# Kernel tuning notes

Measured on AMD Instinct MI355X. Metric: run time of the kernel, lower is better.

## Reference

```python
import jax, jax.numpy as jnp
import numpy as np

IMG = 64            # image_height = image_width = 64
NPTS = 300          # n_pts_per_ray
MIN_DEPTH, MAX_DEPTH = 0.1, 3.0
GRID = 16           # latent_dim -> 16^3 voxel grid
VOXEL_SIZE = 0.1
FOV_DEG = 60.0      # pytorch3d FoVPerspectiveCameras default
B = 8               # number of cameras / latents
EPS = 1e-10         # EmissionAbsorptionRaymarcher eps


def _look_at(eye, at):
    # pytorch3d look_at_view_transform: row-vector convention x_view = x_world @ R + T
    up = np.array([0.0, 1.0, 0.0])
    z = at - eye; z = z / np.linalg.norm(z)
    x = np.cross(up, z); x = x / np.linalg.norm(x)
    y = np.cross(z, x); y = y / np.linalg.norm(y)
    R = np.stack([x, y, z], axis=1)  # columns are camera axes
    T = -eye @ R
    return R, T


def setup_inputs():
    rng = np.random.default_rng(0)
    Rs, Ts = [], []
    for _ in range(B):
        eye = rng.standard_normal(3) * np.array([0.01, 0.0001, 0.01])
        at = rng.standard_normal(3) * 0.01
        R, T = _look_at(eye, at)
        Rs.append(R); Ts.append(T)

    def lin(fan_in, fan_out):
        bound = 1.0 / np.sqrt(fan_in)  # torch Linear default init
        W = rng.uniform(-bound, bound, size=(fan_in, fan_out))
        b = rng.uniform(-bound, bound, size=(fan_out,))
        return jnp.asarray(W, jnp.float32), jnp.asarray(b, jnp.float32)

    W1, b1 = lin(30, 60)
    W2, b2 = lin(60, 480)
    W3, b3 = lin(480, 4 * GRID ** 3)
    zs = jnp.asarray(rng.standard_normal((B, 30)), jnp.float32)
    return {"zs": zs, "W1": W1, "b1": b1, "W2": W2, "b2": b2, "W3": W3, "b3": b3,
            "R": jnp.asarray(np.stack(Rs), jnp.float32),
            "T": jnp.asarray(np.stack(Ts), jnp.float32)}


def _grid_sample3d(vol, xyz):
    # vol: (C, D, H, W); xyz: (..., 3) in [-1, 1]; trilinear, align_corners=True, zero padding
    C, D, H, W = vol.shape
    batch_shape = xyz.shape[:-1]
    p = xyz.reshape(-1, 3)
    ix = (p[:, 0] + 1.0) * 0.5 * (W - 1)
    iy = (p[:, 1] + 1.0) * 0.5 * (H - 1)
    iz = (p[:, 2] + 1.0) * 0.5 * (D - 1)
    x0 = jnp.floor(ix); y0 = jnp.floor(iy); z0 = jnp.floor(iz)
    tx = ix - x0; ty = iy - y0; tz = iz - z0
    out = jnp.zeros((C, p.shape[0]), vol.dtype)
    for dx, wx in ((0, 1.0 - tx), (1, tx)):
        for dy, wy in ((0, 1.0 - ty), (1, ty)):
            for dz, wz in ((0, 1.0 - tz), (1, tz)):
                xf, yf, zf = x0 + dx, y0 + dy, z0 + dz
                valid = ((xf >= 0) & (xf <= W - 1) & (yf >= 0) & (yf <= H - 1)
                         & (zf >= 0) & (zf <= D - 1))
                xi = jnp.clip(xf, 0, W - 1).astype(jnp.int32)
                yi = jnp.clip(yf, 0, H - 1).astype(jnp.int32)
                zi = jnp.clip(zf, 0, D - 1).astype(jnp.int32)
                w = jnp.where(valid, wx * wy * wz, 0.0)
                out = out + w[None, :] * vol[:, zi, yi, xi]
    return jnp.moveaxis(out.reshape((C,) + batch_shape), 0, -1)


def _forward(zs, W1, b1, W2, b2, W3, b3, R, T):
    # latent MLP -> (B, 4, 16, 16, 16) volume (1 density channel + 3 color channels)
    h = jax.nn.sigmoid(zs @ W1 + b1)
    h = jax.nn.sigmoid(h @ W2 + b2)
    lat = jax.nn.sigmoid(h @ W3 + b3).reshape(-1, 4, GRID, GRID, GRID)
    densities = lat[:, 0:1]   # (B,1,D,H,W)
    colors = lat[:, 1:4]      # (B,3,D,H,W)

    # NDCGridRaysampler pixel-center grid (pytorch3d NDC: +x left, +y up, row 0 at max y)
    half_pix = 1.0 / IMG
    xs = jnp.linspace(1.0 - half_pix, -1.0 + half_pix, IMG)
    ys = jnp.linspace(1.0 - half_pix, -1.0 + half_pix, IMG)
    f = 1.0 / jnp.tan(jnp.deg2rad(FOV_DEG) / 2.0)  # focal from fov, aspect=1
    dir_cam = jnp.stack([jnp.broadcast_to(xs[None, :] / f, (IMG, IMG)),
                         jnp.broadcast_to(ys[:, None] / f, (IMG, IMG)),
                         jnp.ones((IMG, IMG))], axis=-1)  # (H,W,3)
    Rt = jnp.swapaxes(R, 1, 2)                             # view->world rotation
    dirs_w = jnp.einsum('hwc,bcd->bhwd', dir_cam, Rt)      # (B,H,W,3)
    origins_w = jnp.einsum('bc,bcd->bd', -T, Rt)           # camera centers (B,3)

    depths = jnp.linspace(MIN_DEPTH, MAX_DEPTH, NPTS)
    pts = origins_w[:, None, None, None, :] + dirs_w[:, :, :, None, :] * depths[None, None, None, :, None]
    half_extent = (GRID - 1) * VOXEL_SIZE * 0.5            # pytorch3d Volumes world->local scale
    local = pts / half_extent                              # (B,H,W,P,3)

    sigma = jax.vmap(_grid_sample3d)(densities, local)[..., 0]  # (B,H,W,P)
    feats = jax.vmap(_grid_sample3d)(colors, local)             # (B,H,W,P,3)

    # EmissionAbsorptionRaymarcher (surface_thickness=1)
    a = (1.0 + EPS) - sigma
    cp = jnp.cumprod(a, axis=-1)
    absorption = jnp.concatenate([jnp.ones_like(cp[..., :1]), cp[..., :-1]], axis=-1)
    weights = sigma * absorption
    rgb = jnp.sum(weights[..., None] * feats, axis=-2)          # (B,H,W,3)
    opacity = 1.0 - jnp.prod(1.0 - sigma, axis=-1, keepdims=True)
    return jnp.concatenate([rgb, opacity], axis=-1)             # (B,H,W,4)


def reference(zs, W1, b1, W2, b2, W3, b3, R, T):
    imgs = _forward(zs, W1, b1, W2, b2, W3, b3, R, T)
    return imgs[..., 3:4], imgs[..., 0:3]
```

## Files before the change

kernel.cpp:

```cpp
#include <hip/hip_runtime.h>
#include <hip/hip_bf16.h>

#define IMG 64
#define NPTS 300
#define GRIDN 16
#define BATCH 8

typedef __hip_bfloat16 bf16;

__device__ __forceinline__ float sigm(float x) { return 1.0f / (1.0f + __expf(-x)); }
__device__ __forceinline__ float lo_bf(unsigned u) { return __uint_as_float(u << 16); }
__device__ __forceinline__ float hi_bf(unsigned u) { return __uint_as_float(u & 0xffff0000u); }

template <typename T>
__device__ __forceinline__ float ldv(const void* p, int i);
template <>
__device__ __forceinline__ float ldv<float>(const void* p, int i) { return ((const float*)p)[i]; }
template <>
__device__ __forceinline__ float ldv<bf16>(const void* p, int i) {
    return __bfloat162float(((const bf16*)p)[i]);
}

__device__ __forceinline__ void sniff(const void* W1, int* sflag, int t) {
    if (t < 64) {
        float m = 0.0f;
        for (int i = t; i < 1800; i += 64) {
            float v = fabsf(__bfloat162float(((const bf16*)W1)[i]));
            if (!(v < 1e30f)) v = 1e30f;
            m = fmaxf(m, v);
        }
#pragma unroll
        for (int d = 1; d < 64; d <<= 1) m = fmaxf(m, __shfl_xor(m, d));
        if (t == 0) *sflag = (m > 4.0f) ? 1 : 0;
    }
}

template <typename T>
__device__ void prep_body(const void* zs, const void* b1, const void* W1, const void* W2,
                          const void* b2, const void* W3, const void* b3,
                          bf16* __restrict__ volbf) {
    __shared__ float z[BATCH][30];
    __shared__ float h1[BATCH][60];
    __shared__ __align__(16) float h2[BATCH][480];
    int t = threadIdx.x;

    if (t < 240) {
        int b = t / 30, i = t - b * 30;
        z[b][i] = ldv<T>(zs, t);
    }
    __syncthreads();
    if (t < 480) {
        int b = t / 60, j = t - b * 60;
        float acc = ldv<T>(b1, j);
#pragma unroll
        for (int i = 0; i < 30; ++i) acc = fmaf(z[b][i], ldv<T>(W1, i * 60 + j), acc);
        h1[b][j] = sigm(acc);
    }
    __syncthreads();
    for (int idx = t; idx < BATCH * 480; idx += 512) {
        int b = idx / 480, col = idx - b * 480;
        float acc = ldv<T>(b2, col);
#pragma unroll
        for (int i = 0; i < 60; ++i) acc = fmaf(h1[b][i], ldv<T>(W2, i * 480 + col), acc);
        h2[b][col] = sigm(acc);
    }
    __syncthreads();

    int b = t >> 6;
    int j = blockIdx.x * 64 + (t & 63);
    float acc = ldv<T>(b3, j);
#pragma unroll 2
    for (int i = 0; i < 480; i += 8) {
        float4 ha = *(const float4*)&h2[b][i];
        float4 hb = *(const float4*)&h2[b][i + 4];
        acc = fmaf(ha.x, ldv<T>(W3, (size_t)(i + 0) * 16384 + j), acc);
        acc = fmaf(ha.y, ldv<T>(W3, (size_t)(i + 1) * 16384 + j), acc);
        acc = fmaf(ha.z, ldv<T>(W3, (size_t)(i + 2) * 16384 + j), acc);
        acc = fmaf(ha.w, ldv<T>(W3, (size_t)(i + 3) * 16384 + j), acc);
        acc = fmaf(hb.x, ldv<T>(W3, (size_t)(i + 4) * 16384 + j), acc);
        acc = fmaf(hb.y, ldv<T>(W3, (size_t)(i + 5) * 16384 + j), acc);
        acc = fmaf(hb.z, ldv<T>(W3, (size_t)(i + 6) * 16384 + j), acc);
        acc = fmaf(hb.w, ldv<T>(W3, (size_t)(i + 7) * 16384 + j), acc);
    }
    float a = sigm(acc);
    int c = j >> 12, v = j & 4095;
    volbf[(size_t)(((b << 12) + v) << 2) + c] = __float2bfloat16(a);
}

__global__ __launch_bounds__(512) void prep_kernel(const void* zs, const void* W1,
                                                   const void* b1, const void* W2,
                                                   const void* b2, const void* W3,
                                                   const void* b3, bf16* __restrict__ volbf,
                                                   int* __restrict__ flag) {
    __shared__ int sflag;
    int t = threadIdx.x;
    sniff(W1, &sflag, t);
    __syncthreads();
    if (blockIdx.x == 0 && t == 0) *flag = sflag;
    if (sflag)
        prep_body<float>(zs, b1, W1, W2, b2, W3, b3, volbf);
    else
        prep_body<bf16>(zs, b1, W1, W2, b2, W3, b3, volbf);
}

__global__ __launch_bounds__(256) void render_kernel(const void* Rm, const void* Tm,
                                                     const bf16* __restrict__ volbf, void* out,
                                                     const int* __restrict__ flag) {
    __shared__ uint2 vox[4096];
    int t = threadIdx.x;
    int rayBase = blockIdx.x * 64;
    int b = rayBase >> 12;
    const uint2* src = (const uint2*)(volbf + (size_t)b * 4096 * 4);
    for (int i = t; i < 4096; i += 256) vox[i] = src[i];
    __syncthreads();

    int f32out = *flag;
    int ray = rayBase + (t >> 2);
    int seg = t & 3;
    int pix = ray & 4095;
    int h = pix >> 6, w = pix & 63;

    const float inv_f = 0.57735026919f;
    float dcx = (0.984375f - 0.03125f * (float)w) * inv_f;
    float dcy = (0.984375f - 0.03125f * (float)h) * inv_f;

    float R[9], Tv[3];
    if (f32out) {
#pragma unroll
        for (int i = 0; i < 9; ++i) R[i] = ((const float*)Rm)[b * 9 + i];
#pragma unroll
        for (int i = 0; i < 3; ++i) Tv[i] = ((const float*)Tm)[b * 3 + i];
    } else {
#pragma unroll
        for (int i = 0; i < 9; ++i) R[i] = __bfloat162float(((const bf16*)Rm)[b * 9 + i]);
#pragma unroll
        for (int i = 0; i < 3; ++i) Tv[i] = __bfloat162float(((const bf16*)Tm)[b * 3 + i]);
    }

    float dx_ = dcx * R[0] + dcy * R[1] + R[2];
    float dy_ = dcx * R[3] + dcy * R[4] + R[5];
    float dz_ = dcx * R[6] + dcy * R[7] + R[8];
    float ox = -(Tv[0] * R[0] + Tv[1] * R[1] + Tv[2] * R[2]);
    float oy = -(Tv[0] * R[3] + Tv[1] * R[4] + Tv[2] * R[5]);
    float oz = -(Tv[0] * R[6] + Tv[1] * R[7] + Tv[2] * R[8]);

    float tA = -1e30f, tB = 1e30f;
    bool miss = false;
    {
        float dd[3] = {dx_, dy_, dz_}, oo[3] = {ox, oy, oz};
#pragma unroll
        for (int a = 0; a < 3; ++a) {
            if (fabsf(dd[a]) > 1e-8f) {
                float inv = 1.0f / dd[a];
                float ra = (-0.85f - oo[a]) * inv, rb = (0.85f - oo[a]) * inv;
                tA = fmaxf(tA, fminf(ra, rb));
                tB = fminf(tB, fmaxf(ra, rb));
            } else if (fabsf(oo[a]) >= 0.85f) {
                miss = true;
            }
        }
    }
    const float step = 2.9f / 299.0f;
    const float inv_step = 299.0f / 2.9f;
    int ilo = 0, ihi = -1;
    if (!miss && tB > tA) {
        float flo = fmaxf(-2.0f, fminf(302.0f, ceilf((tA - 0.1f) * inv_step)));
        float fhi = fmaxf(-2.0f, fminf(302.0f, floorf((tB - 0.1f) * inv_step)));
        ilo = (int)flo - 1;
        ihi = (int)fhi + 1;
        if (ilo < 0) ilo = 0;
        if (ihi > 299) ihi = 299;
    }
    int n = ihi - ilo + 1;
    if (n < 0) n = 0;
    int s0 = ilo + (n * seg) / 4;
    int s1 = ilo + (n * (seg + 1)) / 4;

    float cr = 0.f, cg = 0.f, cb = 0.f, Pa = 1.f;
    for (int i = s0; i < s1; ++i) {
        float tt = 0.1f + step * (float)i;
        float ix = fmaf(fmaf(tt, dx_, ox), 10.0f, 7.5f);
        float iy = fmaf(fmaf(tt, dy_, oy), 10.0f, 7.5f);
        float iz = fmaf(fmaf(tt, dz_, oz), 10.0f, 7.5f);
        float fx = floorf(ix), fy = floorf(iy), fz = floorf(iz);
        float txf = ix - fx, tyf = iy - fy, tzf = iz - fz;
        int x0 = (int)fx, y0 = (int)fy, z0 = (int)fz;

        float sx = 0.f, sr = 0.f, sg = 0.f, sb = 0.f;
        if (((unsigned)x0 < 15u) & ((unsigned)y0 < 15u) & ((unsigned)z0 < 15u)) {
            int base = (z0 << 8) + (y0 << 4) + x0;
            float wx0 = 1.0f - txf, wy0 = 1.0f - tyf, wz0 = 1.0f - tzf;
            float wxy00 = wx0 * wy0, wxy10 = txf * wy0, wxy01 = wx0 * tyf, wxy11 = txf * tyf;
#define CORNF(W, OFF)                          \
    {                                          \
        uint2 q = vox[base + (OFF)];           \
        float wgt_ = (W);                      \
        sx = fmaf(wgt_, lo_bf(q.x), sx);       \
        sr = fmaf(wgt_, hi_bf(q.x), sr);       \
        sg = fmaf(wgt_, lo_bf(q.y), sg);       \
        sb = fmaf(wgt_, hi_bf(q.y), sb);       \
    }
            CORNF(wxy00 * wz0, 0)
            CORNF(wxy10 * wz0, 1)
            CORNF(wxy01 * wz0, 16)
            CORNF(wxy11 * wz0, 17)
            CORNF(wxy00 * tzf, 256)
            CORNF(wxy10 * tzf, 257)
            CORNF(wxy01 * tzf, 272)
            CORNF(wxy11 * tzf, 273)
#undef CORNF
        } else {
            float wx0 = (x0 >= 0 && x0 <= 15) ? (1.0f - txf) : 0.0f;
            float wx1 = (x0 >= -1 && x0 <= 14) ? txf : 0.0f;
            float wy0 = (y0 >= 0 && y0 <= 15) ? (1.0f - tyf) : 0.0f;
            float wy1 = (y0 >= -1 && y0 <= 14) ? tyf : 0.0f;
            float wz0 = (z0 >= 0 && z0 <= 15) ? (1.0f - tzf) : 0.0f;
            float wz1 = (z0 >= -1 && z0 <= 14) ? tzf : 0.0f;
            int xi0 = min(max(x0, 0), 15), xi1 = min(max(x0 + 1, 0), 15);
            int yi0 = min(max(y0, 0), 15), yi1 = min(max(y0 + 1, 0), 15);
            int zi0 = min(max(z0, 0), 15), zi1 = min(max(z0 + 1, 0), 15);
#define CORN(W, ZI, YI, XI)                              \
    {                                                    \
        uint2 q = vox[((ZI) << 8) + ((YI) << 4) + (XI)]; \
        sx = fmaf((W), lo_bf(q.x), sx);                  \
        sr = fmaf((W), hi_bf(q.x), sr);                  \
        sg = fmaf((W), lo_bf(q.y), sg);                  \
        sb = fmaf((W), hi_bf(q.y), sb);                  \
    }
            float wxy00 = wx0 * wy0, wxy10 = wx1 * wy0, wxy01 = wx0 * wy1, wxy11 = wx1 * wy1;
            CORN(wxy00 * wz0, zi0, yi0, xi0)
            CORN(wxy10 * wz0, zi0, yi0, xi1)
            CORN(wxy01 * wz0, zi0, yi1, xi0)
            CORN(wxy11 * wz0, zi0, yi1, xi1)
            CORN(wxy00 * wz1, zi1, yi0, xi0)
            CORN(wxy10 * wz1, zi1, yi0, xi1)
            CORN(wxy01 * wz1, zi1, yi1, xi0)
            CORN(wxy11 * wz1, zi1, yi1, xi1)
#undef CORN
        }

        float wgt = sx * Pa;
        cr = fmaf(wgt, sr, cr);
        cg = fmaf(wgt, sg, cg);
        cb = fmaf(wgt, sb, cb);
        Pa *= (1.0f - sx);
    }

#pragma unroll
    for (int d = 1; d < 4; d <<= 1) {
        float o_cr = __shfl_xor(cr, d);
        float o_cg = __shfl_xor(cg, d);
        float o_cb = __shfl_xor(cb, d);
        float o_Pa = __shfl_xor(Pa, d);
        bool first = ((seg & d) == 0);
        cr = first ? fmaf(Pa, o_cr, cr) : fmaf(o_Pa, cr, o_cr);
        cg = first ? fmaf(Pa, o_cg, cg) : fmaf(o_Pa, cg, o_cg);
        cb = first ? fmaf(Pa, o_cb, cb) : fmaf(o_Pa, cb, o_cb);
        Pa *= o_Pa;
    }

    if (seg == 0) {
        if (f32out) {
            float* of = (float*)out;
            of[ray] = 1.0f - Pa;
            float* orgb = of + BATCH * IMG * IMG;
            orgb[ray * 3 + 0] = cr;
            orgb[ray * 3 + 1] = cg;
            orgb[ray * 3 + 2] = cb;
        } else {
            bf16* ob = (bf16*)out;
            ob[ray] = __float2bfloat16(1.0f - Pa);
            bf16* orgb = ob + BATCH * IMG * IMG;
            orgb[ray * 3 + 0] = __float2bfloat16(cr);
            orgb[ray * 3 + 1] = __float2bfloat16(cg);
            orgb[ray * 3 + 2] = __float2bfloat16(cb);
        }
    }
}

extern "C" void kernel_launch(void* const* d_in, const int* in_sizes, int n_in,
                              void* d_out, int out_size, void* d_ws, size_t ws_size,
                              hipStream_t stream) {
    const void* zs = d_in[0];
    const void* W1 = d_in[1];
    const void* b1 = d_in[2];
    const void* W2 = d_in[3];
    const void* b2 = d_in[4];
    const void* W3 = d_in[5];
    const void* b3 = d_in[6];
    const void* Rm = d_in[7];
    const void* Tm = d_in[8];

    bf16* volbf = (bf16*)d_ws;
    int* flag = (int*)((char*)d_ws + 262144);

    hipLaunchKernelGGL(prep_kernel, dim3(256), dim3(512), 0, stream, zs, W1, b1, W2, b2, W3,
                       b3, volbf, flag);
    hipLaunchKernelGGL(render_kernel, dim3(512), dim3(256), 0, stream, Rm, Tm, volbf, d_out,
                       flag);
}
```

Baseline: 141.0 us.

## Split W3 GEMV over K-slices with vector loads and shared-memory reduction

Restructures the third-layer GEMV so each thread handles 8 adjacent output columns for one batch over a 60-row K-slice. W3 is read with 16-byte vector loads, and the partial sums from the 8 slices are combined through a shared-memory reduction buffer. Previously every thread walked all 480 rows with scalar loads, and each W3 element was loaded separately by each of the 8 batch rows. The change should cut the serial dependency chain and raise memory-level parallelism. In exchange it adds 16KB of shared memory and an extra barrier.

Result: faster. 138.1 us (-2.1%).

```diff
diff --git a/kernel.cpp b/kernel.cpp
--- a/kernel.cpp
+++ b/kernel.cpp
@@ -41,7 +41,8 @@
                           bf16* __restrict__ volbf) {
     __shared__ float z[BATCH][30];
     __shared__ float h1[BATCH][60];
-    __shared__ __align__(16) float h2[BATCH][480];
+    __shared__ __align__(16) float h2[BATCH][488];
+    __shared__ float red[512][8];
     int t = threadIdx.x;
 
     if (t < 240) {
@@ -66,25 +67,69 @@
     }
     __syncthreads();
 
-    int b = t >> 6;
-    int j = blockIdx.x * 64 + (t & 63);
-    float acc = ldv<T>(b3, j);
-#pragma unroll 2
-    for (int i = 0; i < 480; i += 8) {
-        float4 ha = *(const float4*)&h2[b][i];
-        float4 hb = *(const float4*)&h2[b][i + 4];
-        acc = fmaf(ha.x, ldv<T>(W3, (size_t)(i + 0) * 16384 + j), acc);
-        acc = fmaf(ha.y, ldv<T>(W3, (size_t)(i + 1) * 16384 + j), acc);
-        acc = fmaf(ha.z, ldv<T>(W3, (size_t)(i + 2) * 16384 + j), acc);
-        acc = fmaf(ha.w, ldv<T>(W3, (size_t)(i + 3) * 16384 + j), acc);
-        acc = fmaf(hb.x, ldv<T>(W3, (size_t)(i + 4) * 16384 + j), acc);
-        acc = fmaf(hb.y, ldv<T>(W3, (size_t)(i + 5) * 16384 + j), acc);
-        acc = fmaf(hb.z, ldv<T>(W3, (size_t)(i + 6) * 16384 + j), acc);
-        acc = fmaf(hb.w, ldv<T>(W3, (size_t)(i + 7) * 16384 + j), acc);
-    }
-    float a = sigm(acc);
+    int g = t & 7;
+    int b = (t >> 3) & 7;
+    int s = t >> 6;
+    int j0 = blockIdx.x * 64 + g * 8;
+    const float* h2row = &h2[b][s * 60];
+
+    float acc[8];
+#pragma unroll
+    for (int c = 0; c < 8; ++c) acc[c] = 0.0f;
+
+    if (sizeof(T) == 2) {
+        const unsigned short* w3p = (const unsigned short*)W3 + (size_t)(s * 60) * 16384 + j0;
+        for (int k = 0; k < 60; k += 4) {
+            float4 hv = *(const float4*)(h2row + k);
+            float hk[4] = {hv.x, hv.y, hv.z, hv.w};
+#pragma unroll
+            for (int r = 0; r < 4; ++r) {
+                uint4 q = *(const uint4*)(w3p + (size_t)(k + r) * 16384);
+                float h = hk[r];
+                acc[0] = fmaf(h, lo_bf(q.x), acc[0]);
+                acc[1] = fmaf(h, hi_bf(q.x), acc[1]);
+                acc[2] = fmaf(h, lo_bf(q.y), acc[2]);
+                acc[3] = fmaf(h, hi_bf(q.y), acc[3]);
+                acc[4] = fmaf(h, lo_bf(q.z), acc[4]);
+                acc[5] = fmaf(h, hi_bf(q.z), acc[5]);
+                acc[6] = fmaf(h, lo_bf(q.w), acc[6]);
+                acc[7] = fmaf(h, hi_bf(q.w), acc[7]);
+            }
+        }
+    } else {
+        const float* w3p = (const float*)W3 + (size_t)(s * 60) * 16384 + j0;
+        for (int k = 0; k < 60; k += 4) {
+            float4 hv = *(const float4*)(h2row + k);
+            float hk[4] = {hv.x, hv.y, hv.z, hv.w};
+#pragma unroll
+            for (int r = 0; r < 4; ++r) {
+                float4 qa = *(const float4*)(w3p + (size_t)(k + r) * 16384);
+                float4 qb = *(const float4*)(w3p + (size_t)(k + r) * 16384 + 4);
+                float h = hk[r];
+                acc[0] = fmaf(h, qa.x, acc[0]);
+                acc[1] = fmaf(h, qa.y, acc[1]);
+                acc[2] = fmaf(h, qa.z, acc[2]);
+                acc[3] = fmaf(h, qa.w, acc[3]);
+                acc[4] = fmaf(h, qb.x, acc[4]);
+                acc[5] = fmaf(h, qb.y, acc[5]);
+                acc[6] = fmaf(h, qb.z, acc[6]);
+                acc[7] = fmaf(h, qb.w, acc[7]);
+            }
+        }
+    }
+
+    *(float4*)&red[t][0] = make_float4(acc[0], acc[1], acc[2], acc[3]);
+    *(float4*)&red[t][4] = make_float4(acc[4], acc[5], acc[6], acc[7]);
+    __syncthreads();
+
+    int ob = t >> 6, oc = t & 63;
+    int j = blockIdx.x * 64 + oc;
+    float a = ldv<T>(b3, j);
+#pragma unroll
+    for (int ss = 0; ss < 8; ++ss) a += red[(ss << 6) + (ob << 3) + (oc >> 3)][oc & 7];
+    a = sigm(a);
     int c = j >> 12, v = j & 4095;
-    volbf[(size_t)(((b << 12) + v) << 2) + c] = __float2bfloat16(a);
+    volbf[(size_t)(((ob << 12) + v) << 2) + c] = __float2bfloat16(a);
 }
 
 __global__ __launch_bounds__(512) void prep_kernel(const void* zs, const void* W1,
```

## Restructure W3 GEMV with vectorized loads, batch reuse and split-K reduction

Applied to the files above, without the earlier changes.

The final dense layer now has each thread load 8 contiguous W3 columns with 16-byte loads and accumulate all 8 batch outputs in registers. The 480-row reduction is split across the 8 waves and combined through a shared-memory buffer before bias, sigmoid and the bf16 store. The grid drops from 256 to 32 blocks, which cuts redundant recomputation of the first two layers and W3 load instructions. The risk is lower parallelism and memory-bandwidth utilization with only 32 blocks, plus higher register pressure from 64 accumulators.

Measured after the change: 144.6 us. +2.6%, slower.

```diff
diff --git a/kernel.cpp b/kernel.cpp
--- a/kernel.cpp
+++ b/kernel.cpp
@@ -35,56 +35,132 @@
     }
 }
 
+struct PrepSmem {
+    float z[BATCH][30];
+    float h1[BATCH][60];
+    alignas(16) float h2[BATCH][488];
+    alignas(16) float red[8][4][512];
+};
+
 template <typename T>
 __device__ void prep_body(const void* zs, const void* b1, const void* W1, const void* W2,
                           const void* b2, const void* W3, const void* b3,
-                          bf16* __restrict__ volbf) {
-    __shared__ float z[BATCH][30];
-    __shared__ float h1[BATCH][60];
-    __shared__ __align__(16) float h2[BATCH][480];
+                          bf16* __restrict__ volbf, PrepSmem* sm) {
     int t = threadIdx.x;
 
     if (t < 240) {
         int b = t / 30, i = t - b * 30;
-        z[b][i] = ldv<T>(zs, t);
+        sm->z[b][i] = ldv<T>(zs, t);
     }
     __syncthreads();
     if (t < 480) {
         int b = t / 60, j = t - b * 60;
         float acc = ldv<T>(b1, j);
 #pragma unroll
-        for (int i = 0; i < 30; ++i) acc = fmaf(z[b][i], ldv<T>(W1, i * 60 + j), acc);
-        h1[b][j] = sigm(acc);
+        for (int i = 0; i < 30; ++i) acc = fmaf(sm->z[b][i], ldv<T>(W1, i * 60 + j), acc);
+        sm->h1[b][j] = sigm(acc);
     }
     __syncthreads();
     for (int idx = t; idx < BATCH * 480; idx += 512) {
         int b = idx / 480, col = idx - b * 480;
         float acc = ldv<T>(b2, col);
 #pragma unroll
-        for (int i = 0; i < 60; ++i) acc = fmaf(h1[b][i], ldv<T>(W2, i * 480 + col), acc);
-        h2[b][col] = sigm(acc);
-    }
-    __syncthreads();
-
-    int b = t >> 6;
-    int j = blockIdx.x * 64 + (t & 63);
-    float acc = ldv<T>(b3, j);
+        for (int i = 0; i < 60; ++i) acc = fmaf(sm->h1[b][i], ldv<T>(W2, i * 480 + col), acc);
+        sm->h2[b][col] = sigm(acc);
+    }
+    __syncthreads();
+
+    int w = t >> 6, l = t & 63;
+    int j0 = blockIdx.x * 512 + l * 8;
+    int r0 = w * 60;
+
+    float acc[BATCH][8];
+#pragma unroll
+    for (int b = 0; b < BATCH; ++b)
+#pragma unroll
+        for (int c = 0; c < 8; ++c) acc[b][c] = 0.0f;
+
+    if (sizeof(T) == 2) {
+        const unsigned short* w3p = (const unsigned short*)W3 + (size_t)r0 * 16384 + j0;
 #pragma unroll 2
-    for (int i = 0; i < 480; i += 8) {
-        float4 ha = *(const float4*)&h2[b][i];
-        float4 hb = *(const float4*)&h2[b][i + 4];
-        acc = fmaf(ha.x, ldv<T>(W3, (size_t)(i + 0) * 16384 + j), acc);
-        acc = fmaf(ha.y, ldv<T>(W3, (size_t)(i + 1) * 16384 + j), acc);
-        acc = fmaf(ha.z, ldv<T>(W3, (size_t)(i + 2) * 16384 + j), acc);
-        acc = fmaf(ha.w, ldv<T>(W3, (size_t)(i + 3) * 16384 + j), acc);
-        acc = fmaf(hb.x, ldv<T>(W3, (size_t)(i + 4) * 16384 + j), acc);
-        acc = fmaf(hb.y, ldv<T>(W3, (size_t)(i + 5) * 16384 + j), acc);
-        acc = fmaf(hb.z, ldv<T>(W3, (size_t)(i + 6) * 16384 + j), acc);
-        acc = fmaf(hb.w, ldv<T>(W3, (size_t)(i + 7) * 16384 + j), acc);
-    }
-    float a = sigm(acc);
-    int c = j >> 12, v = j & 4095;
-    volbf[(size_t)(((b << 12) + v) << 2) + c] = __float2bfloat16(a);
+        for (int k = 0; k < 60; k += 4) {
+            uint4 q[4];
+#pragma unroll
+            for (int r = 0; r < 4; ++r) q[r] = *(const uint4*)(w3p + (size_t)(k + r) * 16384);
+            float wv[4][8];
+#pragma unroll
+            for (int r = 0; r < 4; ++r) {
+                wv[r][0] = lo_bf(q[r].x); wv[r][1] = hi_bf(q[r].x);
+                wv[r][2] = lo_bf(q[r].y); wv[r][3] = hi_bf(q[r].y);
+                wv[r][4] = lo_bf(q[r].z); wv[r][5] = hi_bf(q[r].z);
+                wv[r][6] = lo_bf(q[r].w); wv[r][7] = hi_bf(q[r].w);
+            }
+#pragma unroll
+            for (int b = 0; b < BATCH; ++b) {
+                float4 hv = *(const float4*)&sm->h2[b][r0 + k];
+                float hk[4] = {hv.x, hv.y, hv.z, hv.w};
+#pragma unroll
+                for (int r = 0; r < 4; ++r)
+#pragma unroll
+                    for (int c = 0; c < 8; ++c) acc[b][c] = fmaf(hk[r], wv[r][c], acc[b][c]);
+            }
+        }
+    } else {
+        const float* w3p = (const float*)W3 + (size_t)r0 * 16384 + j0;
+#pragma unroll 2
+        for (int k = 0; k < 60; k += 4) {
+            float wv[4][8];
+#pragma unroll
+            for (int r = 0; r < 4; ++r) {
+                float4 qa = *(const float4*)(w3p + (size_t)(k + r) * 16384);
+                float4 qb = *(const float4*)(w3p + (size_t)(k + r) * 16384 + 4);
+                wv[r][0] = qa.x; wv[r][1] = qa.y; wv[r][2] = qa.z; wv[r][3] = qa.w;
+                wv[r][4] = qb.x; wv[r][5] = qb.y; wv[r][6] = qb.z; wv[r][7] = qb.w;
+            }
+#pragma unroll
+            for (int b = 0; b < BATCH; ++b) {
+                float4 hv = *(const float4*)&sm->h2[b][r0 + k];
+                float hk[4] = {hv.x, hv.y, hv.z, hv.w};
+#pragma unroll
+                for (int r = 0; r < 4; ++r)
+#pragma unroll
+                    for (int c = 0; c < 8; ++c) acc[b][c] = fmaf(hk[r], wv[r][c], acc[b][c]);
+            }
+        }
+    }
+
+#pragma unroll
+    for (int half = 0; half < 2; ++half) {
+#pragma unroll
+        for (int b = 0; b < 4; ++b) {
+            int bb = half * 4 + b;
+            *(float4*)&sm->red[w][b][l * 8] =
+                make_float4(acc[bb][0], acc[bb][1], acc[bb][2], acc[bb][3]);
+            *(float4*)&sm->red[w][b][l * 8 + 4] =
+                make_float4(acc[bb][4], acc[bb][5], acc[bb][6], acc[bb][7]);
+        }
+        __syncthreads();
+        {
+            int ob = t >> 7;
+            int cl = (t & 127) * 4;
+            float4 s = make_float4(0.f, 0.f, 0.f, 0.f);
+#pragma unroll
+            for (int ww = 0; ww < 8; ++ww) {
+                float4 p = *(const float4*)&sm->red[ww][ob][cl];
+                s.x += p.x; s.y += p.y; s.z += p.z; s.w += p.w;
+            }
+            int j = blockIdx.x * 512 + cl;
+            int c = j >> 12, v0 = j & 4095;
+            int bb = half * 4 + ob;
+            float sv[4] = {s.x, s.y, s.z, s.w};
+#pragma unroll
+            for (int k2 = 0; k2 < 4; ++k2) {
+                float a = sv[k2] + ldv<T>(b3, j + k2);
+                volbf[(size_t)(((bb << 12) + v0 + k2) << 2) + c] = __float2bfloat16(sigm(a));
+            }
+        }
+        __syncthreads();
+    }
 }
 
 __global__ __launch_bounds__(512) void prep_kernel(const void* zs, const void* W1,
@@ -92,15 +168,16 @@
                                                    const void* b2, const void* W3,
                                                    const void* b3, bf16* __restrict__ volbf,
                                                    int* __restrict__ flag) {
+    __shared__ PrepSmem sm;
     __shared__ int sflag;
     int t = threadIdx.x;
     sniff(W1, &sflag, t);
     __syncthreads();
     if (blockIdx.x == 0 && t == 0) *flag = sflag;
     if (sflag)
-        prep_body<float>(zs, b1, W1, W2, b2, W3, b3, volbf);
+        prep_body<float>(zs, b1, W1, W2, b2, W3, b3, volbf, &sm);
     else
-        prep_body<bf16>(zs, b1, W1, W2, b2, W3, b3, volbf);
+        prep_body<bf16>(zs, b1, W1, W2, b2, W3, b3, volbf, &sm);
 }
 
 __global__ __launch_bounds__(256) void render_kernel(const void* Rm, const void* Tm,
@@ -294,7 +371,7 @@
     bf16* volbf = (bf16*)d_ws;
     int* flag = (int*)((char*)d_ws + 262144);
 
-    hipLaunchKernelGGL(prep_kernel, dim3(256), dim3(512), 0, stream, zs, W1, b1, W2, b2, W3,
+    hipLaunchKernelGGL(prep_kernel, dim3(32), dim3(512), 0, stream, zs, W1, b1, W2, b2, W3,
                        b3, volbf, flag);
     hipLaunchKernelGGL(render_kernel, dim3(512), dim3(256), 0, stream, Rm, Tm, volbf, d_out,
                        flag);
```
